# Performance work log

Measured on AMD Instinct MI355X. Metric: run time of the kernel, lower is better.

## Reference

```python
import jax, jax.numpy as jnp
import numpy as np

NEG_SLOPE = 0.2
MASK_FILL = -9e10


def setup_inputs() -> dict:
    key = jax.random.key(0)
    ks = jax.random.split(key, 8)
    B, N, D = 8, 2048, 64
    return {
        "opes_mask_adj": jax.random.randint(ks[0], (B, N, N), 0, 2, dtype=jnp.int32),
        "opes_mask_job": jax.random.randint(ks[1], (B, N, N), 0, 2, dtype=jnp.int32),
        "batch_idxes": jnp.arange(B, dtype=jnp.int64),
        "feats": jax.random.normal(ks[2], (B, N, D), dtype=jnp.float32),
        "W_ope": jax.random.normal(ks[3], (D, D), dtype=jnp.float32) * (1.0 / np.sqrt(D)),
        "attn_src": jax.random.normal(ks[4], (D,), dtype=jnp.float32) * (1.0 / np.sqrt(D)),
        "attn_dst": jax.random.normal(ks[5], (D,), dtype=jnp.float32) * (1.0 / np.sqrt(D)),
        "lambda_params": jax.random.normal(ks[6], (D, 2), dtype=jnp.float32),
    }


def reference(opes_mask_adj, opes_mask_job, batch_idxes, feats, W_ope, attn_src, attn_dst, lambda_params):
    # h_ope: [B, N, D]  (Linear with weight [out,in]: x @ W^T)
    h_ope = jnp.einsum("bnd,od->bno", feats, W_ope)
    a_src = h_ope @ attn_src  # [B, N]
    a_dst = h_ope @ attn_dst  # [B, N]
    e = a_src[:, :, None] + a_dst[:, None, :]  # [B, N, N]
    e = jnp.where(e >= 0, e, NEG_SLOPE * e)  # leaky relu

    mask_adj = opes_mask_adj[batch_idxes] == 1
    alpha_adj = jax.nn.softmax(jnp.where(mask_adj, e, MASK_FILL), axis=-1)
    h_adj = jnp.einsum("bnm,bmd->bnd", alpha_adj, h_ope)

    mask_job = opes_mask_job[batch_idxes] == 1
    alpha_job = jax.nn.softmax(jnp.where(mask_job, e, MASK_FILL), axis=-1)
    h_job = jnp.einsum("bnm,bmd->bnd", alpha_job, h_ope)

    # in_dim == out_dim -> identity residual (res_fc is None)
    lambdas = jax.nn.softmax(lambda_params, axis=1)  # [D, 2]
    lambda_adj, lambda_job = lambdas[:, 0], lambdas[:, 1]
    return lambda_adj * h_adj + lambda_job * h_job + feats
```

## Files before the change

kernel.cpp:

```cpp
#include <hip/hip_runtime.h>
#include <hip/hip_bf16.h>

#define B_ 8
#define N_ 2048
#define D_ 64

typedef __attribute__((ext_vector_type(8))) short bf16x8;
typedef __attribute__((ext_vector_type(4))) float f32x4;

__device__ inline unsigned short f32_bf16_rne(float f) {
    unsigned u = __float_as_uint(f);
    u += 0x7fffu + ((u >> 16) & 1u);
    return (unsigned short)(u >> 16);
}

__global__ __launch_bounds__(256) void prep_kernel(
    const float* __restrict__ feats, const float* __restrict__ W,
    const float* __restrict__ attn_src, const float* __restrict__ attn_dst,
    unsigned short* __restrict__ hT, float* __restrict__ a_src,
    float* __restrict__ a_dst) {
    __shared__ float w_lds[64 * 65];
    __shared__ float f_lds[32 * 64];
    __shared__ unsigned short hT_lds[64 * 40];

    const int t = threadIdx.x;
    const int b = blockIdx.x >> 6;
    const int rowbase = (blockIdx.x & 63) * 32;

#pragma unroll
    for (int k = 0; k < 4; k++) {
        int lin = (k * 256 + t) * 4;
        float4 v = *(const float4*)(W + lin);
        int o = lin >> 6, d = lin & 63;
        float* p = &w_lds[o * 65 + d];
        p[0] = v.x; p[1] = v.y; p[2] = v.z; p[3] = v.w;
    }
#pragma unroll
    for (int k = 0; k < 2; k++) {
        int lin = (k * 256 + t) * 4;
        float4 v = *(const float4*)(feats + (size_t)(b * N_ + rowbase) * D_ + lin);
        float* p = &f_lds[lin];
        p[0] = v.x; p[1] = v.y; p[2] = v.z; p[3] = v.w;
    }
    __syncthreads();

    const int w = t >> 6;
    const int o = t & 63;
    float acc[8] = {0.f, 0.f, 0.f, 0.f, 0.f, 0.f, 0.f, 0.f};
#pragma unroll 8
    for (int d = 0; d < 64; d++) {
        float wv = w_lds[o * 65 + d];
#pragma unroll
        for (int rr = 0; rr < 8; rr++)
            acc[rr] = fmaf(f_lds[(w * 8 + rr) * 64 + d], wv, acc[rr]);
    }
    float as_ = attn_src[o], ad_ = attn_dst[o];
#pragma unroll
    for (int rr = 0; rr < 8; rr++) {
        int row = rowbase + w * 8 + rr;
        float s1 = acc[rr] * as_;
        float s2 = acc[rr] * ad_;
#pragma unroll
        for (int off = 32; off; off >>= 1) {
            s1 += __shfl_xor(s1, off);
            s2 += __shfl_xor(s2, off);
        }
        if (o == 0) {
            a_src[b * N_ + row] = s1;
            a_dst[b * N_ + row] = s2;
        }
        hT_lds[o * 40 + w * 8 + rr] = f32_bf16_rne(acc[rr]);
    }
    __syncthreads();
    const int d = t >> 2, seg = t & 3;
    uint4 vv = *(const uint4*)(&hT_lds[d * 40 + seg * 8]);
    *(uint4*)(hT + ((size_t)(b * 64 + d) * N_ + rowbase + seg * 8)) = vv;
}

__global__ __launch_bounds__(512, 4) void attn_kernel(
    const int* __restrict__ mask_adj, const int* __restrict__ mask_job,
    const int* __restrict__ batch_idxes,
    const unsigned short* __restrict__ hT, const float* __restrict__ a_src,
    const float* __restrict__ a_dst, const float* __restrict__ feats,
    const float* __restrict__ lambda_params, float* __restrict__ out) {
    __shared__ unsigned short hstage[2 * 64 * 128];
    __shared__ float zb[256];

    const int t = threadIdx.x;
    const int b = blockIdx.x >> 6;
    const int ibase = (blockIdx.x & 63) * 64;
    (void)b; (void)ibase;

    const int blk = blockIdx.x;
    const int bb = blk >> 6;
    (void)bb;
    const int batch = blk / 32;
    (void)batch;

    const int b2 = blockIdx.x >> 5;
    const int ib2 = (blockIdx.x & 31) * 64;

    const int wid = t >> 6, lane = t & 63;
    const int rowg = wid & 3;
    const int jh = wid >> 2;
    const int m = lane & 15, q = lane >> 4;
    const int irow0 = ib2 + rowg * 16;
    const int i_a = irow0 + m;

    int bi = batch_idxes[b2];
    bi = (bi < 0) ? 0 : ((bi >= B_) ? (B_ - 1) : bi);
    const int* mA = mask_adj + (size_t)bi * N_ * N_ + (size_t)i_a * N_;
    const int* mJ = mask_job + (size_t)bi * N_ * N_ + (size_t)i_a * N_;
    const float asrc = a_src[b2 * N_ + i_a];
    const float* adst = a_dst + b2 * N_;

    f32x4 accA[4], accJ[4];
#pragma unroll
    for (int dd = 0; dd < 4; dd++) {
        accA[dd] = (f32x4){0.f, 0.f, 0.f, 0.f};
        accJ[dd] = (f32x4){0.f, 0.f, 0.f, 0.f};
    }
    float zA = 0.f, zJ = 0.f;

    const int tt_ = t & 255;
    const int sd = tt_ >> 2, sseg = tt_ & 3;
    const unsigned short* hrow = hT + (size_t)(b2 * 64 + sd) * N_;
    unsigned short* hst = hstage + jh * (64 * 128);

    for (int jt = 0; jt < 8; jt++) {
        const int j0 = jh * 1024 + jt * 128;
#pragma unroll
        for (int c = 0; c < 4; c++) {
            int jc = sseg * 4 + c;
            uint4 v = *(const uint4*)(hrow + j0 + jc * 8);
            *(uint4*)(hst + (sd * 16 + (jc ^ (sd & 15))) * 8) = v;
        }
        __syncthreads();

#pragma unroll
        for (int kk = 0; kk < 4; kk++) {
            const int jl = j0 + kk * 32 + q * 8;
            int4 a0 = *(const int4*)(mA + jl);
            int4 a1 = *(const int4*)(mA + jl + 4);
            int4 b0 = *(const int4*)(mJ + jl);
            int4 b1 = *(const int4*)(mJ + jl + 4);
            float4 d0 = *(const float4*)(adst + jl);
            float4 d1 = *(const float4*)(adst + jl + 4);
            int ma[8] = {a0.x, a0.y, a0.z, a0.w, a1.x, a1.y, a1.z, a1.w};
            int mj[8] = {b0.x, b0.y, b0.z, b0.w, b1.x, b1.y, b1.z, b1.w};
            float dv[8] = {d0.x, d0.y, d0.z, d0.w, d1.x, d1.y, d1.z, d1.w};
            bf16x8 fa, fj;
#pragma unroll
            for (int u = 0; u < 8; u++) {
                float e = asrc + dv[u];
                float le = fmaxf(e, 0.f) + 0.2f * fminf(e, 0.f);
                float p = __expf(le);
                float pa = (ma[u] == 1) ? p : 0.f;
                float pj = (mj[u] == 1) ? p : 0.f;
                zA += pa;
                zJ += pj;
                fa[u] = (short)f32_bf16_rne(pa);
                fj[u] = (short)f32_bf16_rne(pj);
            }
#pragma unroll
            for (int dd = 0; dd < 4; dd++) {
                int dn = dd * 16 + m;
                int jcl = kk * 4 + q;
                bf16x8 fb = *(const bf16x8*)(hst + (dn * 16 + (jcl ^ (dn & 15))) * 8);
                accA[dd] = __builtin_amdgcn_mfma_f32_16x16x32_bf16(fa, fb, accA[dd], 0, 0, 0);
                accJ[dd] = __builtin_amdgcn_mfma_f32_16x16x32_bf16(fj, fb, accJ[dd], 0, 0, 0);
            }
        }
        __syncthreads();
    }

    zA += __shfl_xor(zA, 16); zA += __shfl_xor(zA, 32);
    zJ += __shfl_xor(zJ, 16); zJ += __shfl_xor(zJ, 32);

    __syncthreads();
    float* cbuf = (float*)hstage;
    if (jh == 1) {
#pragma unroll
        for (int dd = 0; dd < 4; dd++)
#pragma unroll
            for (int r = 0; r < 4; r++) {
                cbuf[(rowg * 32 + dd * 4 + r) * 64 + lane] = accA[dd][r];
                cbuf[(rowg * 32 + 16 + dd * 4 + r) * 64 + lane] = accJ[dd][r];
            }
        if (q == 0) {
            zb[128 + rowg * 16 + m] = zA;
            zb[192 + rowg * 16 + m] = zJ;
        }
    } else if (q == 0) {
        zb[rowg * 16 + m] = zA;
        zb[64 + rowg * 16 + m] = zJ;
    }
    __syncthreads();

    if (jh == 0) {
        float invA[4], invJ[4];
#pragma unroll
        for (int r = 0; r < 4; r++) {
            int rw = rowg * 16 + q * 4 + r;
            invA[r] = 1.f / (zb[rw] + zb[128 + rw]);
            invJ[r] = 1.f / (zb[64 + rw] + zb[192 + rw]);
        }
#pragma unroll
        for (int dd = 0; dd < 4; dd++) {
            int d = dd * 16 + m;
            float l0 = lambda_params[d * 2];
            float l1 = lambda_params[d * 2 + 1];
            float e0 = __expf(l0), e1 = __expf(l1);
            float inv = 1.f / (e0 + e1);
            float la = e0 * inv, lj = e1 * inv;
#pragma unroll
            for (int r = 0; r < 4; r++) {
                int i = irow0 + q * 4 + r;
                float vA = accA[dd][r] + cbuf[(rowg * 32 + dd * 4 + r) * 64 + lane];
                float vJ = accJ[dd][r] + cbuf[(rowg * 32 + 16 + dd * 4 + r) * 64 + lane];
                size_t off = (size_t)(b2 * N_ + i) * D_ + d;
                out[off] = la * vA * invA[r] + lj * vJ * invJ[r] + feats[off];
            }
        }
    }
}

extern "C" void kernel_launch(void* const* d_in, const int* in_sizes, int n_in,
                              void* d_out, int out_size, void* d_ws, size_t ws_size,
                              hipStream_t stream) {
    const int* mask_adj = (const int*)d_in[0];
    const int* mask_job = (const int*)d_in[1];
    const int* batch_idxes = (const int*)d_in[2];
    const float* feats = (const float*)d_in[3];
    const float* W = (const float*)d_in[4];
    const float* attn_src = (const float*)d_in[5];
    const float* attn_dst = (const float*)d_in[6];
    const float* lambda_params = (const float*)d_in[7];
    float* out = (float*)d_out;

    unsigned short* hT = (unsigned short*)d_ws;
    float* a_src = (float*)((char*)d_ws + (size_t)B_ * 64 * N_ * 2);
    float* a_dst = a_src + B_ * N_;

    prep_kernel<<<B_ * (N_ / 32), 256, 0, stream>>>(feats, W, attn_src, attn_dst,
                                                    hT, a_src, a_dst);
    attn_kernel<<<B_ * (N_ / 64), 512, 0, stream>>>(mask_adj, mask_job, batch_idxes,
                                                    hT, a_src, a_dst, feats,
                                                    lambda_params, out);
}
```

Baseline: 322.1 us.

## Split attention key range four ways with 1024-thread blocks

Each attention block now runs 16 waves instead of 8. The 2048-column key range is split into four quarter slices of 512 columns, each handled by its own group of four waves, which halves each wave's serial loop. Partial accumulators and softmax denominators are combined through LDS in a two-step tree reduction before the final epilogue. The aim is more memory-level parallelism and latency hiding for the mask stream on a grid that has only one block per CU. The cost is a doubled LDS staging buffer, extra barriers, and a tighter register budget per thread at 1024 threads.

```diff
diff --git a/kernel.cpp b/kernel.cpp
--- a/kernel.cpp
+++ b/kernel.cpp
@@ -77,32 +77,22 @@
     *(uint4*)(hT + ((size_t)(b * 64 + d) * N_ + rowbase + seg * 8)) = vv;
 }
 
-__global__ __launch_bounds__(512, 4) void attn_kernel(
+__global__ __launch_bounds__(1024) void attn_kernel(
     const int* __restrict__ mask_adj, const int* __restrict__ mask_job,
     const int* __restrict__ batch_idxes,
     const unsigned short* __restrict__ hT, const float* __restrict__ a_src,
     const float* __restrict__ a_dst, const float* __restrict__ feats,
     const float* __restrict__ lambda_params, float* __restrict__ out) {
-    __shared__ unsigned short hstage[2 * 64 * 128];
-    __shared__ float zb[256];
+    __shared__ unsigned short hstage[4 * 64 * 128];
+    __shared__ float zb[512];
 
     const int t = threadIdx.x;
-    const int b = blockIdx.x >> 6;
-    const int ibase = (blockIdx.x & 63) * 64;
-    (void)b; (void)ibase;
-
-    const int blk = blockIdx.x;
-    const int bb = blk >> 6;
-    (void)bb;
-    const int batch = blk / 32;
-    (void)batch;
-
     const int b2 = blockIdx.x >> 5;
     const int ib2 = (blockIdx.x & 31) * 64;
 
     const int wid = t >> 6, lane = t & 63;
     const int rowg = wid & 3;
-    const int jh = wid >> 2;
+    const int jq = wid >> 2;
     const int m = lane & 15, q = lane >> 4;
     const int irow0 = ib2 + rowg * 16;
     const int i_a = irow0 + m;
@@ -122,13 +112,13 @@
     }
     float zA = 0.f, zJ = 0.f;
 
-    const int tt_ = t & 255;
-    const int sd = tt_ >> 2, sseg = tt_ & 3;
+    const int lt = t & 255;
+    const int sd = lt >> 2, sseg = lt & 3;
     const unsigned short* hrow = hT + (size_t)(b2 * 64 + sd) * N_;
-    unsigned short* hst = hstage + jh * (64 * 128);
-
-    for (int jt = 0; jt < 8; jt++) {
-        const int j0 = jh * 1024 + jt * 128;
+    unsigned short* hst = hstage + jq * (64 * 128);
+
+    for (int jt = 0; jt < 4; jt++) {
+        const int j0 = jq * 512 + jt * 128;
 #pragma unroll
         for (int c = 0; c < 4; c++) {
             int jc = sseg * 4 + c;
@@ -177,33 +167,54 @@
     zA += __shfl_xor(zA, 16); zA += __shfl_xor(zA, 32);
     zJ += __shfl_xor(zJ, 16); zJ += __shfl_xor(zJ, 32);
 
-    __syncthreads();
     float* cbuf = (float*)hstage;
-    if (jh == 1) {
+    if (jq >= 2) {
 #pragma unroll
         for (int dd = 0; dd < 4; dd++)
 #pragma unroll
             for (int r = 0; r < 4; r++) {
-                cbuf[(rowg * 32 + dd * 4 + r) * 64 + lane] = accA[dd][r];
-                cbuf[(rowg * 32 + 16 + dd * 4 + r) * 64 + lane] = accJ[dd][r];
-            }
-        if (q == 0) {
-            zb[128 + rowg * 16 + m] = zA;
-            zb[192 + rowg * 16 + m] = zJ;
-        }
-    } else if (q == 0) {
-        zb[rowg * 16 + m] = zA;
-        zb[64 + rowg * 16 + m] = zJ;
-    }
-    __syncthreads();
-
-    if (jh == 0) {
+                int blkb = ((jq - 2) * 4 + rowg) * 32;
+                cbuf[(blkb + dd * 4 + r) * 64 + lane] = accA[dd][r];
+                cbuf[(blkb + 16 + dd * 4 + r) * 64 + lane] = accJ[dd][r];
+            }
+    }
+    if (q == 0) {
+        zb[jq * 128 + rowg * 16 + m] = zA;
+        zb[jq * 128 + 64 + rowg * 16 + m] = zJ;
+    }
+    __syncthreads();
+
+    if (jq <= 1) {
+#pragma unroll
+        for (int dd = 0; dd < 4; dd++)
+#pragma unroll
+            for (int r = 0; r < 4; r++) {
+                int blkb = (jq * 4 + rowg) * 32;
+                accA[dd][r] += cbuf[(blkb + dd * 4 + r) * 64 + lane];
+                accJ[dd][r] += cbuf[(blkb + 16 + dd * 4 + r) * 64 + lane];
+            }
+    }
+    __syncthreads();
+
+    if (jq == 1) {
+#pragma unroll
+        for (int dd = 0; dd < 4; dd++)
+#pragma unroll
+            for (int r = 0; r < 4; r++) {
+                int blkb = rowg * 32;
+                cbuf[(blkb + dd * 4 + r) * 64 + lane] = accA[dd][r];
+                cbuf[(blkb + 16 + dd * 4 + r) * 64 + lane] = accJ[dd][r];
+            }
+    }
+    __syncthreads();
+
+    if (jq == 0) {
         float invA[4], invJ[4];
 #pragma unroll
         for (int r = 0; r < 4; r++) {
             int rw = rowg * 16 + q * 4 + r;
-            invA[r] = 1.f / (zb[rw] + zb[128 + rw]);
-            invJ[r] = 1.f / (zb[64 + rw] + zb[192 + rw]);
+            invA[r] = 1.f / (zb[rw] + zb[128 + rw] + zb[256 + rw] + zb[384 + rw]);
+            invJ[r] = 1.f / (zb[64 + rw] + zb[192 + rw] + zb[320 + rw] + zb[448 + rw]);
         }
 #pragma unroll
         for (int dd = 0; dd < 4; dd++) {
@@ -213,11 +224,12 @@
             float e0 = __expf(l0), e1 = __expf(l1);
             float inv = 1.f / (e0 + e1);
             float la = e0 * inv, lj = e1 * inv;
+            int blkb = rowg * 32;
 #pragma unroll
             for (int r = 0; r < 4; r++) {
                 int i = irow0 + q * 4 + r;
-                float vA = accA[dd][r] + cbuf[(rowg * 32 + dd * 4 + r) * 64 + lane];
-                float vJ = accJ[dd][r] + cbuf[(rowg * 32 + 16 + dd * 4 + r) * 64 + lane];
+                float vA = accA[dd][r] + cbuf[(blkb + dd * 4 + r) * 64 + lane];
+                float vJ = accJ[dd][r] + cbuf[(blkb + 16 + dd * 4 + r) * 64 + lane];
                 size_t off = (size_t)(b2 * N_ + i) * D_ + d;
                 out[off] = la * vA * invA[r] + lj * vJ * invJ[r] + feats[off];
             }
@@ -244,7 +256,7 @@
 
     prep_kernel<<<B_ * (N_ / 32), 256, 0, stream>>>(feats, W, attn_src, attn_dst,
                                                     hT, a_src, a_dst);
-    attn_kernel<<<B_ * (N_ / 64), 512, 0, stream>>>(mask_adj, mask_job, batch_idxes,
-                                                    hT, a_src, a_dst, feats,
-                                                    lambda_params, out);
-}
+    attn_kernel<<<B_ * (N_ / 64), 1024, 0, stream>>>(mask_adj, mask_job, batch_idxes,
+                                                     hT, a_src, a_dst, feats,
+                                                     lambda_params, out);
+}
```

After: 322.2 us. No clear change (+0.0%).
